# Kernel optimization log

Measured on AMD Instinct MI355X. Metric: run time of the kernel, lower is better.

The kernel has to match this reference:

```python
import jax, jax.numpy as jnp
import numpy as np

N, T, H, D = 8, 192, 1024, 128
P = 4            # t_patch_size (kernel = stride)
TP = T // P      # 48 patch tokens
E = 16384
HOUR, WDAY = 48, 7


def conv1d_patch(e, W, b):
    # e: [B, Cin, T]; W: [Cout, Cin, P]; kernel == stride == P (non-overlapping)
    B, Ci, Tt = e.shape
    e = e.reshape(B, Ci, Tt // P, P)
    return jnp.einsum('bctk,ock->bot', e, W) + b[None, :, None]  # [B, Cout, T']


def gcn_propagate(x, src, dst, coef):
    # x: [B, H, D] ; symmetric-normalized sparse A_hat @ x
    msg = x[:, src, :] * coef[None, :, None]
    return jnp.zeros_like(x).at[:, dst, :].add(msg)


def setup_inputs() -> dict:
    key = jax.random.key(0)
    ks = jax.random.split(key, 12)
    x = jax.random.normal(ks[0], (N, 1, T, H, 1), dtype=jnp.float32)
    x_mark = jax.random.randint(ks[1], (N, T, 2), 0, 7).astype(jnp.int64)
    edges = jax.random.randint(ks[2], (E, 2), 0, H).astype(jnp.int64)
    node_split = jnp.arange(H, dtype=jnp.int64).reshape(4, 256)
    s = 0.02
    params = {
        'hour_emb': jax.random.normal(ks[3], (HOUR, D), jnp.float32) * s,
        'weekday_emb': jax.random.normal(ks[4], (WDAY, D), jnp.float32) * s,
        'timeconv_w': jax.random.normal(ks[5], (D, D, P), jnp.float32) * s,
        'timeconv_b': jnp.zeros((D,), jnp.float32),
        'tconv_w': jax.random.normal(ks[6], (D, 1, P), jnp.float32) * s,
        'tconv_b': jnp.zeros((D,), jnp.float32),
        'W1': jax.random.normal(ks[7], (D, D), jnp.float32) * s,
        'b1': jnp.zeros((D,), jnp.float32),
        'W2': jax.random.normal(ks[8], (D, D), jnp.float32) * s,
        'b2': jnp.zeros((D,), jnp.float32),
    }
    return dict(x=x, x_mark=x_mark, edges=edges, node_split=node_split, **params)


def reference(x, x_mark, edges, node_split, hour_emb, weekday_emb,
              timeconv_w, timeconv_b, tconv_w, tconv_b, W1, b1, W2, b2):
    # ---- TimeEmb (TemporalEmbedding, hour_num='48') ----
    hour_x = hour_emb[x_mark[:, :, 1]]        # [N, T, D]
    wday_x = weekday_emb[x_mark[:, :, 0]]     # [N, T, D]
    time_emb = conv1d_patch((hour_x + wday_x).transpose(0, 2, 1),
                            timeconv_w, timeconv_b).transpose(0, 2, 1)  # [N, T', D]

    # ---- temporal value embedding ----
    xv = jnp.squeeze(x, (1, 4)).transpose(0, 2, 1).reshape(N * H, 1, T)  # [N*H,1,T]
    tv = conv1d_patch(xv, tconv_w, tconv_b)                 # [N*H, D, T']
    tv = tv.transpose(0, 2, 1).reshape(N, H, TP, D)         # [N, H, T', D]
    tv = tv.transpose(0, 2, 1, 3).reshape(N * TP, H, D)     # [N*T', H, D]

    # ---- 2-layer GCN with self-loops + symmetric normalization ----
    src = jnp.concatenate([edges[:, 0], jnp.arange(H)])
    dst = jnp.concatenate([edges[:, 1], jnp.arange(H)])
    deg = jnp.zeros((H,), tv.dtype).at[dst].add(1.0)
    coef = jax.lax.rsqrt(deg[src] * deg[dst])
    h = jax.nn.relu(gcn_propagate(tv, src, dst, coef) @ W1 + b1)
    token = gcn_propagate(h, src, dst, coef) @ W2 + b2      # [N*T', H, D]
    token = token.reshape(N, TP, H, D)

    # ---- per-group gather + mean pooling, interleaved per time step ----
    G = node_split.shape[0]
    grouped = token[:, :, node_split.reshape(-1), :].reshape(N, TP, G, -1, D)
    token = grouped.mean(axis=3).reshape(N, TP * G, D)      # [N, T'*G, D]

    time_rep = jnp.repeat(time_emb, G, axis=1)              # [N, T'*G, D]
    out = token + time_rep  # is_time == 1; eval mode -> no dropout
    return out, time_rep
```

## Files before the change

kernel.cpp:

```cpp
#include <hip/hip_runtime.h>
#include <hip/hip_bf16.h>

#define NN 8
#define TT 192
#define HH 1024
#define DD 128
#define TPP 48
#define EE 16384
#define NEDGE (EE + HH)
#define BB (NN * TPP)
#define NOUT (NN * TT * DD)

typedef short bf16x8 __attribute__((ext_vector_type(8)));
typedef float f32x4 __attribute__((ext_vector_type(4)));

__device__ __forceinline__ float bf2f(__hip_bfloat16 h) { return __bfloat162float(h); }
__device__ __forceinline__ float us2f(unsigned short u) {
  union { unsigned i; float f; } t;
  t.i = ((unsigned)u) << 16;
  return t.f;
}

__global__ __launch_bounds__(256) void k_setup(
    const int* __restrict__ edges, int* __restrict__ degE,
    const int* __restrict__ node_split, int* __restrict__ inv,
    const float* __restrict__ tw, float* __restrict__ twT,
    float* __restrict__ zbuf,
    const float* __restrict__ x, __hip_bfloat16* __restrict__ Xall) {
  __shared__ float tile[64][65];
  int tid = threadIdx.x, bid = blockIdx.x;
  int i = bid * 256 + tid;
  if (i < EE) atomicAdd(&degE[edges[2 * i + 1]], 1);
  if (i < HH) inv[node_split[i]] = i;
  if (i < 65536) twT[(i & 511) * DD + (i >> 9)] = tw[i];
  if (i < 6144) zbuf[i] = 0.f;

  int tt = bid % 24, st = bid / 24;
  int t0 = tt * 64, s0 = st * 64;
  int sl = tid & 63, r4 = tid >> 6;
#pragma unroll 4
  for (int ii = 0; ii < 16; ++ii) {
    int tl = ii * 4 + r4;
    tile[tl][sl] = x[(size_t)(t0 + tl) * HH + s0 + sl];
  }
  __syncthreads();
#pragma unroll 4
  for (int ii = 0; ii < 16; ++ii) {
    int sl2 = ii * 4 + r4;
    Xall[(size_t)(s0 + sl2) * 1536 + t0 + sl] = __float2bfloat16(tile[sl][sl2]);
  }
}

__global__ __launch_bounds__(1024) void k_scan(const int* __restrict__ degE,
                                               int* __restrict__ row_ptr,
                                               const float* __restrict__ tcw,
                                               const float* __restrict__ tcb,
                                               const float* __restrict__ W1,
                                               float* __restrict__ CW,
                                               const float* __restrict__ W2,
                                               __hip_bfloat16* __restrict__ w2sw) {
  int t = threadIdx.x, lane = t & 63, wid = t >> 6;
  int v = degE[t] + 1;
#pragma unroll
  for (int off = 1; off < 64; off <<= 1) {
    int u = __shfl_up(v, off, 64);
    if (lane >= off) v += u;
  }
  __shared__ int wsum[16];
  if (lane == 63) wsum[wid] = v;
  __syncthreads();
  if (t < 64) {
    int s = (lane < 16) ? wsum[lane] : 0;
#pragma unroll
    for (int off = 1; off < 16; off <<= 1) {
      int u = __shfl_up(s, off, 64);
      if (lane >= off) s += u;
    }
    if (lane < 16) wsum[lane] = s;
  }
  __syncthreads();
  int base = wid ? wsum[wid - 1] : 0;
  row_ptr[t + 1] = base + v;
  if (t == 0) row_ptr[0] = 0;

  if (t < 640) {
    int j = t >> 7, o = t & 127;
    float acc = 0.f;
    if (j < 4)
      for (int d = 0; d < DD; ++d) acc = fmaf(tcw[d * 4 + j], W1[d * DD + o], acc);
    else
      for (int d = 0; d < DD; ++d) acc = fmaf(tcb[d], W1[d * DD + o], acc);
    CW[j * DD + o] = acc;
  }
#pragma unroll 4
  for (int u = 0; u < 16; ++u) {
    int i = t * 16 + u;
    int n = i >> 7, k = i & 127;
    int dstb = n * 256 + (((k >> 3) ^ (n & 7)) * 16) + (k & 7) * 2;
    w2sw[dstb >> 1] = __float2bfloat16(W2[k * DD + n]);
  }
}

__global__ void k_scatter(const int* __restrict__ edges, const int* __restrict__ degE,
                          const int* __restrict__ row_ptr, const int* __restrict__ inv,
                          int* __restrict__ fill, int* __restrict__ csr_src,
                          float* __restrict__ csr_coef, float* __restrict__ csum,
                          float* __restrict__ QT) {
  int e = blockIdx.x * 256 + threadIdx.x;
  if (e >= NEDGE) return;
  int s, dt;
  if (e < EE) { s = edges[2 * e]; dt = edges[2 * e + 1]; }
  else        { s = dt = e - EE; }
  float ds = (float)(degE[s] + 1);
  float dd = (float)(degE[dt] + 1);
  float cf = rsqrtf(ds * dd);
  int pos = atomicAdd(&fill[dt], 1);
  int at = row_ptr[dt] + pos;
  csr_src[at] = s;
  csr_coef[at] = cf;
  atomicAdd(&csum[dt], cf);
  int g = inv[dt] >> 8;
  atomicAdd(&QT[s * 4 + g], cf * (1.0f / 256.0f));
}

__global__ __launch_bounds__(256) void k_spmm(
    const int* __restrict__ row_ptr, const int* __restrict__ csr_src,
    const float* __restrict__ csr_coef, const __hip_bfloat16* __restrict__ Xall,
    __hip_bfloat16* __restrict__ xbar,
    const int* __restrict__ xm, const float* __restrict__ hour_emb,
    const float* __restrict__ wday_emb, const float* __restrict__ twT,
    const float* __restrict__ tcb, float* __restrict__ out) {
  __shared__ float sL[2][512];
  int tid = threadIdx.x, bid = blockIdx.x;
  if (bid < HH) {
    int h = bid;
    int j0 = row_ptr[h], j1 = row_ptr[h + 1];
    float a0 = 0.f, a1 = 0.f, a2 = 0.f, a3 = 0.f, a4 = 0.f, a5 = 0.f;
    for (int j = j0; j < j1; ++j) {
      int s = csr_src[j];
      float cf = csr_coef[j];
      const unsigned* xr = (const unsigned*)(Xall + (size_t)s * 1536);
      unsigned u0 = xr[tid], u1 = xr[tid + 256], u2 = xr[tid + 512];
      union { unsigned i; float f; } lo, hi;
      lo.i = u0 << 16; hi.i = u0 & 0xffff0000u;
      a0 = fmaf(cf, lo.f, a0); a1 = fmaf(cf, hi.f, a1);
      lo.i = u1 << 16; hi.i = u1 & 0xffff0000u;
      a2 = fmaf(cf, lo.f, a2); a3 = fmaf(cf, hi.f, a3);
      lo.i = u2 << 16; hi.i = u2 & 0xffff0000u;
      a4 = fmaf(cf, lo.f, a4); a5 = fmaf(cf, hi.f, a5);
    }
    unsigned* xw = (unsigned*)(xbar + (size_t)h * 1536);
    union { __hip_bfloat16 h2[2]; unsigned u; } pk;
    pk.h2[0] = __float2bfloat16(a0); pk.h2[1] = __float2bfloat16(a1);
    xw[tid] = pk.u;
    pk.h2[0] = __float2bfloat16(a2); pk.h2[1] = __float2bfloat16(a3);
    xw[tid + 256] = pk.u;
    pk.h2[0] = __float2bfloat16(a4); pk.h2[1] = __float2bfloat16(a5);
    xw[tid + 512] = pk.u;
  } else {
    int bb = bid - HH;
    int half = tid >> 7, o = tid & 127;
    int b = bb * 2 + half;
    int n = b / TPP, tp = b % TPP;
    for (int k = 0; k < 4; ++k) {
      int t = tp * 4 + k;
      int wd = xm[(n * TT + t) * 2 + 0];
      int hr = xm[(n * TT + t) * 2 + 1];
      sL[half][o * 4 + k] = hour_emb[hr * DD + o] + wday_emb[wd * DD + o];
    }
    __syncthreads();
    float a0 = tcb[o], a1 = 0.f, a2 = 0.f, a3 = 0.f;
    for (int j = 0; j < 512; j += 4) {
      a0 = fmaf(sL[half][j + 0], twT[(j + 0) * DD + o], a0);
      a1 = fmaf(sL[half][j + 1], twT[(j + 1) * DD + o], a1);
      a2 = fmaf(sL[half][j + 2], twT[(j + 2) * DD + o], a2);
      a3 = fmaf(sL[half][j + 3], twT[(j + 3) * DD + o], a3);
    }
    float acc = (a0 + a1) + (a2 + a3);
    size_t base = (size_t)NOUT + ((size_t)n * TT + tp * 4) * DD + o;
    out[base] = acc;
    out[base + DD] = acc;
    out[base + 2 * DD] = acc;
    out[base + 3 * DD] = acc;
  }
}

__global__ __launch_bounds__(256) void k_red(const __hip_bfloat16* __restrict__ xbar,
                                             const float* __restrict__ csum,
                                             const float* __restrict__ QT,
                                             const float* __restrict__ CW,
                                             const float* __restrict__ b1,
                                             float* __restrict__ ypar) {
  __shared__ float4 xb4[256];
  __shared__ float4 qv[256];
  __shared__ float csv[256];
  __shared__ float yL[512];
  int tid = threadIdx.x, bid = blockIdx.x;
  int b = bid >> 2, qt = bid & 3;
  int h = qt * 256 + tid;
  {
    ushort4 us = *(const ushort4*)(xbar + (size_t)h * 1536 + b * 4);
    xb4[tid] = make_float4(us2f(us.x), us2f(us.y), us2f(us.z), us2f(us.w));
    qv[tid] = *(const float4*)(QT + h * 4);
    csv[tid] = csum[h];
  }
  int o = tid & 127, sub = tid >> 7;
  float cw0 = CW[o], cw1 = CW[DD + o], cw2 = CW[2 * DD + o];
  float cw3 = CW[3 * DD + o], cw4 = CW[4 * DD + o];
  float b1o = b1[o];
  __syncthreads();
  float y0 = 0.f, y1 = 0.f, y2 = 0.f, y3 = 0.f;
  int hh0 = sub * 128;
#pragma unroll 4
  for (int hh = hh0; hh < hh0 + 128; ++hh) {
    float4 xv = xb4[hh];
    float4 q = qv[hh];
    float c = csv[hh];
    float t = fmaf(c, cw4, b1o);
    t = fmaf(xv.x, cw0, t);
    t = fmaf(xv.y, cw1, t);
    t = fmaf(xv.z, cw2, t);
    t = fmaf(xv.w, cw3, t);
    t = fmaxf(t, 0.f);
    y0 = fmaf(q.x, t, y0);
    y1 = fmaf(q.y, t, y1);
    y2 = fmaf(q.z, t, y2);
    y3 = fmaf(q.w, t, y3);
  }
  if (sub == 0) {
    yL[o] = y0; yL[DD + o] = y1; yL[2 * DD + o] = y2; yL[3 * DD + o] = y3;
  }
  __syncthreads();
  if (sub == 1) {
    yL[o] += y0; yL[DD + o] += y1; yL[2 * DD + o] += y2; yL[3 * DD + o] += y3;
  }
  __syncthreads();
  float* yp = ypar + ((size_t)qt * BB + b) * 512;
  yp[tid] = yL[tid];
  yp[tid + 256] = yL[tid + 256];
}

__global__ __launch_bounds__(256, 2) void k_out(const float* __restrict__ ypar,
                                                const __hip_bfloat16* __restrict__ w2sw,
                                                const float* __restrict__ b2,
                                                float* __restrict__ out) {
  __shared__ __align__(16) char Wr[32768];
  __shared__ __align__(16) char Gr[16384];
  int tid = threadIdx.x;
  int m0 = blockIdx.x * 64;
  {
    const uint4* ws = (const uint4*)w2sw;
    uint4* wd = (uint4*)Wr;
    for (int i = tid; i < 2048; i += 256) wd[i] = ws[i];
  }
#pragma unroll 4
  for (int it = 0; it < 16; ++it) {
    int pi = it * 256 + tid;
    int row = pi >> 6, kp = pi & 63;
    int base = (m0 + row) * 128 + 2 * kp;
    float s0 = 0.f, s1 = 0.f;
#pragma unroll
    for (int p = 0; p < 4; ++p) {
      s0 += ypar[(size_t)p * (BB * 512) + base];
      s1 += ypar[(size_t)p * (BB * 512) + base + 1];
    }
    union { __hip_bfloat16 h[2]; unsigned u; } pk;
    pk.h[0] = __float2bfloat16(s0);
    pk.h[1] = __float2bfloat16(s1);
    *(unsigned*)(Gr + row * 256 + (((kp >> 2) ^ (row & 7)) * 16) + (kp & 3) * 4) = pk.u;
  }
  int lane = tid & 63, w = tid >> 6;
  int colq = lane & 15, quad = lane >> 4;
  float bo[8];
#pragma unroll
  for (int jn = 0; jn < 8; ++jn) bo[jn] = b2[jn * 16 + colq];
  __syncthreads();

  f32x4 acc[8];
#pragma unroll
  for (int jn = 0; jn < 8; ++jn) acc[jn] = (f32x4){0.f, 0.f, 0.f, 0.f};
  int arow = w * 16 + colq;
#pragma unroll
  for (int kc = 0; kc < 4; ++kc) {
    bf16x8 af = *(const bf16x8*)(Gr + arow * 256 + (((kc * 4 + quad) ^ (arow & 7)) * 16));
#pragma unroll
    for (int jn = 0; jn < 8; ++jn) {
      int nr = jn * 16 + colq;
      bf16x8 bf = *(const bf16x8*)(Wr + nr * 256 + (((kc * 4 + quad) ^ (nr & 7)) * 16));
      acc[jn] = __builtin_amdgcn_mfma_f32_16x16x32_bf16(af, bf, acc[jn], 0, 0, 0);
    }
  }
#pragma unroll
  for (int reg = 0; reg < 4; ++reg) {
    int m = m0 + w * 16 + quad * 4 + reg;
    int b = m >> 2, g = m & 3;
    int n_ = b / TPP, tp = b % TPP;
    size_t rb = ((size_t)(n_ * TT + tp * 4 + g)) * DD;
#pragma unroll
    for (int jn = 0; jn < 8; ++jn) {
      int o = jn * 16 + colq;
      out[rb + o] = acc[jn][reg] + bo[jn] + out[(size_t)NOUT + rb + o];
    }
  }
}

extern "C" void kernel_launch(void* const* d_in, const int* in_sizes, int n_in,
                              void* d_out, int out_size, void* d_ws, size_t ws_size,
                              hipStream_t stream) {
  const float* x = (const float*)d_in[0];
  const int* xm = (const int*)d_in[1];
  const int* edges = (const int*)d_in[2];
  const int* node_split = (const int*)d_in[3];
  const float* hour_emb = (const float*)d_in[4];
  const float* wday_emb = (const float*)d_in[5];
  const float* timeconv_w = (const float*)d_in[6];
  const float* timeconv_b = (const float*)d_in[7];
  const float* tcw = (const float*)d_in[8];
  const float* tcb = (const float*)d_in[9];
  const float* W1 = (const float*)d_in[10];
  const float* b1 = (const float*)d_in[11];
  const float* W2 = (const float*)d_in[12];
  const float* b2 = (const float*)d_in[13];
  float* out = (float*)d_out;

  char* w = (char*)d_ws;
  int* degE = (int*)(w + 0);
  int* fill = (int*)(w + 4096);
  float* csum = (float*)(w + 8192);
  float* QT = (float*)(w + 12288);
  int* row_ptr = (int*)(w + 28672);
  int* inv = (int*)(w + 33024);
  int* csr_src = (int*)(w + 37120);
  float* csr_coef = (float*)(w + 106752);
  __hip_bfloat16* w2sw = (__hip_bfloat16*)(w + 176384);
  float* CW = (float*)(w + 209152);
  float* twT = (float*)(w + 213248);
  __hip_bfloat16* Xall = (__hip_bfloat16*)(w + 475392);
  float* ypar = (float*)(w + 475392);
  __hip_bfloat16* xbar = (__hip_bfloat16*)(w + 3621120);

  hipMemsetAsync(degE, 0, 4096, stream);
  k_setup<<<384, 256, 0, stream>>>(edges, degE, node_split, inv, timeconv_w, twT,
                                   (float*)(w + 4096), x, Xall);
  k_scan<<<1, 1024, 0, stream>>>(degE, row_ptr, tcw, tcb, W1, CW, W2, w2sw);
  k_scatter<<<68, 256, 0, stream>>>(edges, degE, row_ptr, inv, fill, csr_src, csr_coef,
                                    csum, QT);
  k_spmm<<<HH + BB / 2, 256, 0, stream>>>(row_ptr, csr_src, csr_coef, Xall, xbar, xm,
                                          hour_emb, wday_emb, twT, timeconv_b, out);
  k_red<<<BB * 4, 256, 0, stream>>>(xbar, csum, QT, CW, b1, ypar);
  k_out<<<24, 256, 0, stream>>>(ypar, w2sw, b2, out);
}
```

Baseline: 154.0 us.

## Fuse all stages into one persistent kernel with software grid barriers

Replaces the six kernel launches with a single persistent kernel of 512 blocks. The former kernel boundaries become a hierarchical atomic grid barrier, which is meant to remove launch overhead and the tail idle time between stages. Work is redistributed over the fixed grid: the scan now runs in one 256-thread block, each spmm block handles two nodes, and each reduction block loops over three units. This relies on all 512 blocks being co-resident (launch_bounds 256,2 with 48KB shared memory), otherwise the barrier deadlocks. ypar also moves out of the region it previously shared with Xall.

```diff
diff --git a/kernel.cpp b/kernel.cpp
--- a/kernel.cpp
+++ b/kernel.cpp
@@ -10,296 +10,315 @@
 #define NEDGE (EE + HH)
 #define BB (NN * TPP)
 #define NOUT (NN * TT * DD)
+#define NBLK 512
 
 typedef short bf16x8 __attribute__((ext_vector_type(8)));
 typedef float f32x4 __attribute__((ext_vector_type(4)));
 
-__device__ __forceinline__ float bf2f(__hip_bfloat16 h) { return __bfloat162float(h); }
+struct KParams {
+  const float* x; const int* xm; const int* edges; const int* node_split;
+  const float* hour_emb; const float* wday_emb; const float* tw; const float* tw_b;
+  const float* tcw; const float* tcb; const float* W1; const float* b1;
+  const float* W2; const float* b2;
+  float* out;
+  int* degE; int* bar; float* zbuf; float* csum; float* QT;
+  int* row_ptr; int* inv; int* csr_src; float* csr_coef; int* fill;
+  __hip_bfloat16* w2sw; float* CW; float* twT;
+  __hip_bfloat16* Xall; __hip_bfloat16* xbar; float* ypar;
+};
+
 __device__ __forceinline__ float us2f(unsigned short u) {
   union { unsigned i; float f; } t;
   t.i = ((unsigned)u) << 16;
   return t.f;
 }
 
-__global__ __launch_bounds__(256) void k_setup(
-    const int* __restrict__ edges, int* __restrict__ degE,
-    const int* __restrict__ node_split, int* __restrict__ inv,
-    const float* __restrict__ tw, float* __restrict__ twT,
-    float* __restrict__ zbuf,
-    const float* __restrict__ x, __hip_bfloat16* __restrict__ Xall) {
-  __shared__ float tile[64][65];
-  int tid = threadIdx.x, bid = blockIdx.x;
-  int i = bid * 256 + tid;
-  if (i < EE) atomicAdd(&degE[edges[2 * i + 1]], 1);
-  if (i < HH) inv[node_split[i]] = i;
-  if (i < 65536) twT[(i & 511) * DD + (i >> 9)] = tw[i];
-  if (i < 6144) zbuf[i] = 0.f;
-
-  int tt = bid % 24, st = bid / 24;
-  int t0 = tt * 64, s0 = st * 64;
-  int sl = tid & 63, r4 = tid >> 6;
+__device__ __forceinline__ void gridbar(int* bar) {
+  __syncthreads();
+  if (threadIdx.x == 0) {
+    __threadfence();
+    int gen = __hip_atomic_load(&bar[0], __ATOMIC_RELAXED, __HIP_MEMORY_SCOPE_AGENT);
+    int sub = blockIdx.x & 63;
+    int t = atomicAdd(&bar[32 + sub * 16], 1);
+    if (t == (NBLK / 64) - 1) {
+      atomicExch(&bar[32 + sub * 16], 0);
+      int m = atomicAdd(&bar[16], 1);
+      if (m == 63) {
+        atomicExch(&bar[16], 0);
+        atomicAdd(&bar[0], 1);
+      } else {
+        while (__hip_atomic_load(&bar[0], __ATOMIC_RELAXED, __HIP_MEMORY_SCOPE_AGENT) == gen)
+          __builtin_amdgcn_s_sleep(1);
+      }
+    } else {
+      while (__hip_atomic_load(&bar[0], __ATOMIC_RELAXED, __HIP_MEMORY_SCOPE_AGENT) == gen)
+        __builtin_amdgcn_s_sleep(1);
+    }
+    __threadfence();
+  }
+  __syncthreads();
+}
+
+__global__ __launch_bounds__(256, 2) void k_mega(KParams P) {
+  __shared__ __align__(16) char U[49152];
+  int tid = threadIdx.x;
+  int bid = blockIdx.x;
+
+  if (bid < 256) {
+    int i = bid * 256 + tid;
+    if (i < EE) atomicAdd(&P.degE[P.edges[2 * i + 1]], 1);
+    if (i < HH) P.inv[P.node_split[i]] = i;
+    P.twT[(i & 511) * DD + (i >> 9)] = P.tw[i];
+    if (i < 6144) P.zbuf[i] = 0.f;
+  }
+  if (bid < 384) {
+    float(*tile)[65] = (float(*)[65])U;
+    int tt = bid % 24, st = bid / 24;
+    int t0 = tt * 64, s0 = st * 64;
+    int sl = tid & 63, r4 = tid >> 6;
 #pragma unroll 4
-  for (int ii = 0; ii < 16; ++ii) {
-    int tl = ii * 4 + r4;
-    tile[tl][sl] = x[(size_t)(t0 + tl) * HH + s0 + sl];
-  }
-  __syncthreads();
+    for (int ii = 0; ii < 16; ++ii) {
+      int tl = ii * 4 + r4;
+      tile[tl][sl] = P.x[(size_t)(t0 + tl) * HH + s0 + sl];
+    }
+    __syncthreads();
 #pragma unroll 4
-  for (int ii = 0; ii < 16; ++ii) {
-    int sl2 = ii * 4 + r4;
-    Xall[(size_t)(s0 + sl2) * 1536 + t0 + sl] = __float2bfloat16(tile[sl][sl2]);
-  }
-}
-
-__global__ __launch_bounds__(1024) void k_scan(const int* __restrict__ degE,
-                                               int* __restrict__ row_ptr,
-                                               const float* __restrict__ tcw,
-                                               const float* __restrict__ tcb,
-                                               const float* __restrict__ W1,
-                                               float* __restrict__ CW,
-                                               const float* __restrict__ W2,
-                                               __hip_bfloat16* __restrict__ w2sw) {
-  int t = threadIdx.x, lane = t & 63, wid = t >> 6;
-  int v = degE[t] + 1;
-#pragma unroll
-  for (int off = 1; off < 64; off <<= 1) {
-    int u = __shfl_up(v, off, 64);
-    if (lane >= off) v += u;
-  }
-  __shared__ int wsum[16];
-  if (lane == 63) wsum[wid] = v;
-  __syncthreads();
-  if (t < 64) {
-    int s = (lane < 16) ? wsum[lane] : 0;
-#pragma unroll
-    for (int off = 1; off < 16; off <<= 1) {
-      int u = __shfl_up(s, off, 64);
-      if (lane >= off) s += u;
-    }
-    if (lane < 16) wsum[lane] = s;
-  }
-  __syncthreads();
-  int base = wid ? wsum[wid - 1] : 0;
-  row_ptr[t + 1] = base + v;
-  if (t == 0) row_ptr[0] = 0;
-
-  if (t < 640) {
-    int j = t >> 7, o = t & 127;
-    float acc = 0.f;
-    if (j < 4)
-      for (int d = 0; d < DD; ++d) acc = fmaf(tcw[d * 4 + j], W1[d * DD + o], acc);
-    else
-      for (int d = 0; d < DD; ++d) acc = fmaf(tcb[d], W1[d * DD + o], acc);
-    CW[j * DD + o] = acc;
-  }
-#pragma unroll 4
-  for (int u = 0; u < 16; ++u) {
-    int i = t * 16 + u;
-    int n = i >> 7, k = i & 127;
-    int dstb = n * 256 + (((k >> 3) ^ (n & 7)) * 16) + (k & 7) * 2;
-    w2sw[dstb >> 1] = __float2bfloat16(W2[k * DD + n]);
-  }
-}
-
-__global__ void k_scatter(const int* __restrict__ edges, const int* __restrict__ degE,
-                          const int* __restrict__ row_ptr, const int* __restrict__ inv,
-                          int* __restrict__ fill, int* __restrict__ csr_src,
-                          float* __restrict__ csr_coef, float* __restrict__ csum,
-                          float* __restrict__ QT) {
-  int e = blockIdx.x * 256 + threadIdx.x;
-  if (e >= NEDGE) return;
-  int s, dt;
-  if (e < EE) { s = edges[2 * e]; dt = edges[2 * e + 1]; }
-  else        { s = dt = e - EE; }
-  float ds = (float)(degE[s] + 1);
-  float dd = (float)(degE[dt] + 1);
-  float cf = rsqrtf(ds * dd);
-  int pos = atomicAdd(&fill[dt], 1);
-  int at = row_ptr[dt] + pos;
-  csr_src[at] = s;
-  csr_coef[at] = cf;
-  atomicAdd(&csum[dt], cf);
-  int g = inv[dt] >> 8;
-  atomicAdd(&QT[s * 4 + g], cf * (1.0f / 256.0f));
-}
-
-__global__ __launch_bounds__(256) void k_spmm(
-    const int* __restrict__ row_ptr, const int* __restrict__ csr_src,
-    const float* __restrict__ csr_coef, const __hip_bfloat16* __restrict__ Xall,
-    __hip_bfloat16* __restrict__ xbar,
-    const int* __restrict__ xm, const float* __restrict__ hour_emb,
-    const float* __restrict__ wday_emb, const float* __restrict__ twT,
-    const float* __restrict__ tcb, float* __restrict__ out) {
-  __shared__ float sL[2][512];
-  int tid = threadIdx.x, bid = blockIdx.x;
-  if (bid < HH) {
-    int h = bid;
-    int j0 = row_ptr[h], j1 = row_ptr[h + 1];
-    float a0 = 0.f, a1 = 0.f, a2 = 0.f, a3 = 0.f, a4 = 0.f, a5 = 0.f;
-    for (int j = j0; j < j1; ++j) {
-      int s = csr_src[j];
-      float cf = csr_coef[j];
-      const unsigned* xr = (const unsigned*)(Xall + (size_t)s * 1536);
-      unsigned u0 = xr[tid], u1 = xr[tid + 256], u2 = xr[tid + 512];
-      union { unsigned i; float f; } lo, hi;
-      lo.i = u0 << 16; hi.i = u0 & 0xffff0000u;
-      a0 = fmaf(cf, lo.f, a0); a1 = fmaf(cf, hi.f, a1);
-      lo.i = u1 << 16; hi.i = u1 & 0xffff0000u;
-      a2 = fmaf(cf, lo.f, a2); a3 = fmaf(cf, hi.f, a3);
-      lo.i = u2 << 16; hi.i = u2 & 0xffff0000u;
-      a4 = fmaf(cf, lo.f, a4); a5 = fmaf(cf, hi.f, a5);
-    }
-    unsigned* xw = (unsigned*)(xbar + (size_t)h * 1536);
-    union { __hip_bfloat16 h2[2]; unsigned u; } pk;
-    pk.h2[0] = __float2bfloat16(a0); pk.h2[1] = __float2bfloat16(a1);
-    xw[tid] = pk.u;
-    pk.h2[0] = __float2bfloat16(a2); pk.h2[1] = __float2bfloat16(a3);
-    xw[tid + 256] = pk.u;
-    pk.h2[0] = __float2bfloat16(a4); pk.h2[1] = __float2bfloat16(a5);
-    xw[tid + 512] = pk.u;
-  } else {
-    int bb = bid - HH;
+    for (int ii = 0; ii < 16; ++ii) {
+      int sl2 = ii * 4 + r4;
+      P.Xall[(size_t)(s0 + sl2) * 1536 + t0 + sl] = __float2bfloat16(tile[sl][sl2]);
+    }
+  }
+  gridbar(P.bar);
+
+  if (bid == 0) {
+    int t4 = tid * 4;
+    int v0 = P.degE[t4] + 1, v1 = P.degE[t4 + 1] + 1;
+    int v2 = P.degE[t4 + 2] + 1, v3 = P.degE[t4 + 3] + 1;
+    int s_ = v0 + v1 + v2 + v3;
+    int lane = tid & 63, wid = tid >> 6;
+    int inc = s_;
+#pragma unroll
+    for (int off = 1; off < 64; off <<= 1) {
+      int u = __shfl_up(inc, off, 64);
+      if (lane >= off) inc += u;
+    }
+    int* wsum = (int*)U;
+    if (lane == 63) wsum[wid] = inc;
+    __syncthreads();
+    int wb = 0;
+    for (int ww = 0; ww < wid; ++ww) wb += wsum[ww];
+    int ex = wb + inc - s_;
+    P.row_ptr[t4 + 1] = ex + v0;
+    P.row_ptr[t4 + 2] = ex + v0 + v1;
+    P.row_ptr[t4 + 3] = ex + v0 + v1 + v2;
+    P.row_ptr[t4 + 4] = ex + s_;
+    if (tid == 0) P.row_ptr[0] = 0;
+  } else if (bid <= 192) {
+    int u = bid - 1;
+    float(*sL)[512] = (float(*)[512])U;
     int half = tid >> 7, o = tid & 127;
-    int b = bb * 2 + half;
+    int b = u * 2 + half;
     int n = b / TPP, tp = b % TPP;
     for (int k = 0; k < 4; ++k) {
       int t = tp * 4 + k;
-      int wd = xm[(n * TT + t) * 2 + 0];
-      int hr = xm[(n * TT + t) * 2 + 1];
-      sL[half][o * 4 + k] = hour_emb[hr * DD + o] + wday_emb[wd * DD + o];
-    }
-    __syncthreads();
-    float a0 = tcb[o], a1 = 0.f, a2 = 0.f, a3 = 0.f;
+      int wd = P.xm[(n * TT + t) * 2 + 0];
+      int hr = P.xm[(n * TT + t) * 2 + 1];
+      sL[half][o * 4 + k] = P.hour_emb[hr * DD + o] + P.wday_emb[wd * DD + o];
+    }
+    __syncthreads();
+    float a0 = P.tw_b[o], a1 = 0.f, a2 = 0.f, a3 = 0.f;
     for (int j = 0; j < 512; j += 4) {
-      a0 = fmaf(sL[half][j + 0], twT[(j + 0) * DD + o], a0);
-      a1 = fmaf(sL[half][j + 1], twT[(j + 1) * DD + o], a1);
-      a2 = fmaf(sL[half][j + 2], twT[(j + 2) * DD + o], a2);
-      a3 = fmaf(sL[half][j + 3], twT[(j + 3) * DD + o], a3);
+      a0 = fmaf(sL[half][j + 0], P.twT[(j + 0) * DD + o], a0);
+      a1 = fmaf(sL[half][j + 1], P.twT[(j + 1) * DD + o], a1);
+      a2 = fmaf(sL[half][j + 2], P.twT[(j + 2) * DD + o], a2);
+      a3 = fmaf(sL[half][j + 3], P.twT[(j + 3) * DD + o], a3);
     }
     float acc = (a0 + a1) + (a2 + a3);
     size_t base = (size_t)NOUT + ((size_t)n * TT + tp * 4) * DD + o;
-    out[base] = acc;
-    out[base + DD] = acc;
-    out[base + 2 * DD] = acc;
-    out[base + 3 * DD] = acc;
-  }
-}
-
-__global__ __launch_bounds__(256) void k_red(const __hip_bfloat16* __restrict__ xbar,
-                                             const float* __restrict__ csum,
-                                             const float* __restrict__ QT,
-                                             const float* __restrict__ CW,
-                                             const float* __restrict__ b1,
-                                             float* __restrict__ ypar) {
-  __shared__ float4 xb4[256];
-  __shared__ float4 qv[256];
-  __shared__ float csv[256];
-  __shared__ float yL[512];
-  int tid = threadIdx.x, bid = blockIdx.x;
-  int b = bid >> 2, qt = bid & 3;
-  int h = qt * 256 + tid;
+    P.out[base] = acc;
+    P.out[base + DD] = acc;
+    P.out[base + 2 * DD] = acc;
+    P.out[base + 3 * DD] = acc;
+  } else if (bid <= 195) {
+    int j = (bid - 193) * 256 + tid;
+    if (j < 640) {
+      int jr = j >> 7, o = j & 127;
+      float acc = 0.f;
+      if (jr < 4)
+        for (int d = 0; d < DD; ++d) acc = fmaf(P.tcw[d * 4 + jr], P.W1[d * DD + o], acc);
+      else
+        for (int d = 0; d < DD; ++d) acc = fmaf(P.tcb[d], P.W1[d * DD + o], acc);
+      P.CW[jr * DD + o] = acc;
+    }
+  } else if (bid < 260) {
+    int i = (bid - 196) * 256 + tid;
+    int n = i >> 7, k = i & 127;
+    int dstb = n * 256 + (((k >> 3) ^ (n & 7)) * 16) + (k & 7) * 2;
+    P.w2sw[dstb >> 1] = __float2bfloat16(P.W2[k * DD + n]);
+  }
+  gridbar(P.bar);
+
+  if (bid < 68) {
+    int e = bid * 256 + tid;
+    if (e < NEDGE) {
+      int s, dt;
+      if (e < EE) { s = P.edges[2 * e]; dt = P.edges[2 * e + 1]; }
+      else        { s = dt = e - EE; }
+      float ds = (float)(P.degE[s] + 1);
+      float dd = (float)(P.degE[dt] + 1);
+      float cf = rsqrtf(ds * dd);
+      int pos = atomicAdd(&P.fill[dt], 1);
+      int at = P.row_ptr[dt] + pos;
+      P.csr_src[at] = s;
+      P.csr_coef[at] = cf;
+      atomicAdd(&P.csum[dt], cf);
+      int g = P.inv[dt] >> 8;
+      atomicAdd(&P.QT[s * 4 + g], cf * (1.0f / 256.0f));
+    }
+  }
+  gridbar(P.bar);
+
   {
-    ushort4 us = *(const ushort4*)(xbar + (size_t)h * 1536 + b * 4);
-    xb4[tid] = make_float4(us2f(us.x), us2f(us.y), us2f(us.z), us2f(us.w));
-    qv[tid] = *(const float4*)(QT + h * 4);
-    csv[tid] = csum[h];
-  }
-  int o = tid & 127, sub = tid >> 7;
-  float cw0 = CW[o], cw1 = CW[DD + o], cw2 = CW[2 * DD + o];
-  float cw3 = CW[3 * DD + o], cw4 = CW[4 * DD + o];
-  float b1o = b1[o];
-  __syncthreads();
-  float y0 = 0.f, y1 = 0.f, y2 = 0.f, y3 = 0.f;
-  int hh0 = sub * 128;
+    int h = bid * 2 + (tid >> 7);
+    int c = tid & 127;
+    int j0 = P.row_ptr[h], j1 = P.row_ptr[h + 1];
+    float a[12];
+#pragma unroll
+    for (int u = 0; u < 12; ++u) a[u] = 0.f;
+    for (int j = j0; j < j1; ++j) {
+      int s = P.csr_src[j];
+      float cf = P.csr_coef[j];
+      const unsigned* xr = (const unsigned*)(P.Xall + (size_t)s * 1536);
+#pragma unroll
+      for (int u = 0; u < 6; ++u) {
+        unsigned v = xr[c + u * 128];
+        union { unsigned i; float f; } lo, hi;
+        lo.i = v << 16;
+        hi.i = v & 0xffff0000u;
+        a[2 * u] = fmaf(cf, lo.f, a[2 * u]);
+        a[2 * u + 1] = fmaf(cf, hi.f, a[2 * u + 1]);
+      }
+    }
+    unsigned* xw = (unsigned*)(P.xbar + (size_t)h * 1536);
+#pragma unroll
+    for (int u = 0; u < 6; ++u) {
+      union { __hip_bfloat16 h2[2]; unsigned u2; } pk;
+      pk.h2[0] = __float2bfloat16(a[2 * u]);
+      pk.h2[1] = __float2bfloat16(a[2 * u + 1]);
+      xw[c + u * 128] = pk.u2;
+    }
+  }
+  gridbar(P.bar);
+
+  for (int uu = 0; uu < 3; ++uu) {
+    int unit = bid + uu * NBLK;
+    int b = unit >> 2, qt = unit & 3;
+    int h = qt * 256 + tid;
+    float4* xb4 = (float4*)U;
+    float4* qv = (float4*)(U + 4096);
+    float* csv = (float*)(U + 8192);
+    float* yL = (float*)(U + 9216);
+    {
+      ushort4 us = *(const ushort4*)(P.xbar + (size_t)h * 1536 + b * 4);
+      xb4[tid] = make_float4(us2f(us.x), us2f(us.y), us2f(us.z), us2f(us.w));
+      qv[tid] = *(const float4*)(P.QT + h * 4);
+      csv[tid] = P.csum[h];
+    }
+    int o = tid & 127, sub = tid >> 7;
+    float cw0 = P.CW[o], cw1 = P.CW[DD + o], cw2 = P.CW[2 * DD + o];
+    float cw3 = P.CW[3 * DD + o], cw4 = P.CW[4 * DD + o];
+    float b1o = P.b1[o];
+    __syncthreads();
+    float y0 = 0.f, y1 = 0.f, y2 = 0.f, y3 = 0.f;
+    int hh0 = sub * 128;
 #pragma unroll 4
-  for (int hh = hh0; hh < hh0 + 128; ++hh) {
-    float4 xv = xb4[hh];
-    float4 q = qv[hh];
-    float c = csv[hh];
-    float t = fmaf(c, cw4, b1o);
-    t = fmaf(xv.x, cw0, t);
-    t = fmaf(xv.y, cw1, t);
-    t = fmaf(xv.z, cw2, t);
-    t = fmaf(xv.w, cw3, t);
-    t = fmaxf(t, 0.f);
-    y0 = fmaf(q.x, t, y0);
-    y1 = fmaf(q.y, t, y1);
-    y2 = fmaf(q.z, t, y2);
-    y3 = fmaf(q.w, t, y3);
-  }
-  if (sub == 0) {
-    yL[o] = y0; yL[DD + o] = y1; yL[2 * DD + o] = y2; yL[3 * DD + o] = y3;
-  }
-  __syncthreads();
-  if (sub == 1) {
-    yL[o] += y0; yL[DD + o] += y1; yL[2 * DD + o] += y2; yL[3 * DD + o] += y3;
-  }
-  __syncthreads();
-  float* yp = ypar + ((size_t)qt * BB + b) * 512;
-  yp[tid] = yL[tid];
-  yp[tid + 256] = yL[tid + 256];
-}
-
-__global__ __launch_bounds__(256, 2) void k_out(const float* __restrict__ ypar,
-                                                const __hip_bfloat16* __restrict__ w2sw,
-                                                const float* __restrict__ b2,
-                                                float* __restrict__ out) {
-  __shared__ __align__(16) char Wr[32768];
-  __shared__ __align__(16) char Gr[16384];
-  int tid = threadIdx.x;
-  int m0 = blockIdx.x * 64;
-  {
-    const uint4* ws = (const uint4*)w2sw;
-    uint4* wd = (uint4*)Wr;
-    for (int i = tid; i < 2048; i += 256) wd[i] = ws[i];
-  }
+    for (int hh = hh0; hh < hh0 + 128; ++hh) {
+      float4 xv = xb4[hh];
+      float4 q = qv[hh];
+      float cc = csv[hh];
+      float t = fmaf(cc, cw4, b1o);
+      t = fmaf(xv.x, cw0, t);
+      t = fmaf(xv.y, cw1, t);
+      t = fmaf(xv.z, cw2, t);
+      t = fmaf(xv.w, cw3, t);
+      t = fmaxf(t, 0.f);
+      y0 = fmaf(q.x, t, y0);
+      y1 = fmaf(q.y, t, y1);
+      y2 = fmaf(q.z, t, y2);
+      y3 = fmaf(q.w, t, y3);
+    }
+    if (sub == 0) {
+      yL[o] = y0; yL[DD + o] = y1; yL[2 * DD + o] = y2; yL[3 * DD + o] = y3;
+    }
+    __syncthreads();
+    if (sub == 1) {
+      yL[o] += y0; yL[DD + o] += y1; yL[2 * DD + o] += y2; yL[3 * DD + o] += y3;
+    }
+    __syncthreads();
+    float* yp = P.ypar + ((size_t)qt * BB + b) * 512;
+    yp[tid] = yL[tid];
+    yp[tid + 256] = yL[tid + 256];
+    __syncthreads();
+  }
+  gridbar(P.bar);
+
+  if (bid < 24) {
+    char* Wr = U;
+    char* Gr = U + 32768;
+    int m0 = bid * 64;
+    {
+      const uint4* ws = (const uint4*)P.w2sw;
+      uint4* wd = (uint4*)Wr;
+      for (int i = tid; i < 2048; i += 256) wd[i] = ws[i];
+    }
 #pragma unroll 4
-  for (int it = 0; it < 16; ++it) {
-    int pi = it * 256 + tid;
-    int row = pi >> 6, kp = pi & 63;
-    int base = (m0 + row) * 128 + 2 * kp;
-    float s0 = 0.f, s1 = 0.f;
-#pragma unroll
-    for (int p = 0; p < 4; ++p) {
-      s0 += ypar[(size_t)p * (BB * 512) + base];
-      s1 += ypar[(size_t)p * (BB * 512) + base + 1];
-    }
-    union { __hip_bfloat16 h[2]; unsigned u; } pk;
-    pk.h[0] = __float2bfloat16(s0);
-    pk.h[1] = __float2bfloat16(s1);
-    *(unsigned*)(Gr + row * 256 + (((kp >> 2) ^ (row & 7)) * 16) + (kp & 3) * 4) = pk.u;
-  }
-  int lane = tid & 63, w = tid >> 6;
-  int colq = lane & 15, quad = lane >> 4;
-  float bo[8];
-#pragma unroll
-  for (int jn = 0; jn < 8; ++jn) bo[jn] = b2[jn * 16 + colq];
-  __syncthreads();
-
-  f32x4 acc[8];
-#pragma unroll
-  for (int jn = 0; jn < 8; ++jn) acc[jn] = (f32x4){0.f, 0.f, 0.f, 0.f};
-  int arow = w * 16 + colq;
-#pragma unroll
-  for (int kc = 0; kc < 4; ++kc) {
-    bf16x8 af = *(const bf16x8*)(Gr + arow * 256 + (((kc * 4 + quad) ^ (arow & 7)) * 16));
-#pragma unroll
-    for (int jn = 0; jn < 8; ++jn) {
-      int nr = jn * 16 + colq;
-      bf16x8 bf = *(const bf16x8*)(Wr + nr * 256 + (((kc * 4 + quad) ^ (nr & 7)) * 16));
-      acc[jn] = __builtin_amdgcn_mfma_f32_16x16x32_bf16(af, bf, acc[jn], 0, 0, 0);
-    }
-  }
-#pragma unroll
-  for (int reg = 0; reg < 4; ++reg) {
-    int m = m0 + w * 16 + quad * 4 + reg;
-    int b = m >> 2, g = m & 3;
-    int n_ = b / TPP, tp = b % TPP;
-    size_t rb = ((size_t)(n_ * TT + tp * 4 + g)) * DD;
-#pragma unroll
-    for (int jn = 0; jn < 8; ++jn) {
-      int o = jn * 16 + colq;
-      out[rb + o] = acc[jn][reg] + bo[jn] + out[(size_t)NOUT + rb + o];
+    for (int it = 0; it < 16; ++it) {
+      int pi = it * 256 + tid;
+      int row = pi >> 6, kp = pi & 63;
+      int base = (m0 + row) * 128 + 2 * kp;
+      float s0 = 0.f, s1 = 0.f;
+#pragma unroll
+      for (int p = 0; p < 4; ++p) {
+        s0 += P.ypar[(size_t)p * (BB * 512) + base];
+        s1 += P.ypar[(size_t)p * (BB * 512) + base + 1];
+      }
+      union { __hip_bfloat16 h[2]; unsigned u; } pk;
+      pk.h[0] = __float2bfloat16(s0);
+      pk.h[1] = __float2bfloat16(s1);
+      *(unsigned*)(Gr + row * 256 + (((kp >> 2) ^ (row & 7)) * 16) + (kp & 3) * 4) = pk.u;
+    }
+    int lane = tid & 63, w = tid >> 6;
+    int colq = lane & 15, quad = lane >> 4;
+    float bo[8];
+#pragma unroll
+    for (int jn = 0; jn < 8; ++jn) bo[jn] = P.b2[jn * 16 + colq];
+    __syncthreads();
+
+    f32x4 acc[8];
+#pragma unroll
+    for (int jn = 0; jn < 8; ++jn) acc[jn] = (f32x4){0.f, 0.f, 0.f, 0.f};
+    int arow = w * 16 + colq;
+#pragma unroll
+    for (int kc = 0; kc < 4; ++kc) {
+      bf16x8 af = *(const bf16x8*)(Gr + arow * 256 + (((kc * 4 + quad) ^ (arow & 7)) * 16));
+#pragma unroll
+      for (int jn = 0; jn < 8; ++jn) {
+        int nr = jn * 16 + colq;
+        bf16x8 bf = *(const bf16x8*)(Wr + nr * 256 + (((kc * 4 + quad) ^ (nr & 7)) * 16));
+        acc[jn] = __builtin_amdgcn_mfma_f32_16x16x32_bf16(af, bf, acc[jn], 0, 0, 0);
+      }
+    }
+#pragma unroll
+    for (int reg = 0; reg < 4; ++reg) {
+      int m = m0 + w * 16 + quad * 4 + reg;
+      int b = m >> 2, g = m & 3;
+      int n_ = b / TPP, tp = b % TPP;
+      size_t rb = ((size_t)(n_ * TT + tp * 4 + g)) * DD;
+#pragma unroll
+      for (int jn = 0; jn < 8; ++jn) {
+        int o = jn * 16 + colq;
+        P.out[rb + o] = acc[jn][reg] + bo[jn] + P.out[(size_t)NOUT + rb + o];
+      }
     }
   }
 }
@@ -307,46 +326,41 @@
 extern "C" void kernel_launch(void* const* d_in, const int* in_sizes, int n_in,
                               void* d_out, int out_size, void* d_ws, size_t ws_size,
                               hipStream_t stream) {
-  const float* x = (const float*)d_in[0];
-  const int* xm = (const int*)d_in[1];
-  const int* edges = (const int*)d_in[2];
-  const int* node_split = (const int*)d_in[3];
-  const float* hour_emb = (const float*)d_in[4];
-  const float* wday_emb = (const float*)d_in[5];
-  const float* timeconv_w = (const float*)d_in[6];
-  const float* timeconv_b = (const float*)d_in[7];
-  const float* tcw = (const float*)d_in[8];
-  const float* tcb = (const float*)d_in[9];
-  const float* W1 = (const float*)d_in[10];
-  const float* b1 = (const float*)d_in[11];
-  const float* W2 = (const float*)d_in[12];
-  const float* b2 = (const float*)d_in[13];
-  float* out = (float*)d_out;
-
   char* w = (char*)d_ws;
-  int* degE = (int*)(w + 0);
-  int* fill = (int*)(w + 4096);
-  float* csum = (float*)(w + 8192);
-  float* QT = (float*)(w + 12288);
-  int* row_ptr = (int*)(w + 28672);
-  int* inv = (int*)(w + 33024);
-  int* csr_src = (int*)(w + 37120);
-  float* csr_coef = (float*)(w + 106752);
-  __hip_bfloat16* w2sw = (__hip_bfloat16*)(w + 176384);
-  float* CW = (float*)(w + 209152);
-  float* twT = (float*)(w + 213248);
-  __hip_bfloat16* Xall = (__hip_bfloat16*)(w + 475392);
-  float* ypar = (float*)(w + 475392);
-  __hip_bfloat16* xbar = (__hip_bfloat16*)(w + 3621120);
-
-  hipMemsetAsync(degE, 0, 4096, stream);
-  k_setup<<<384, 256, 0, stream>>>(edges, degE, node_split, inv, timeconv_w, twT,
-                                   (float*)(w + 4096), x, Xall);
-  k_scan<<<1, 1024, 0, stream>>>(degE, row_ptr, tcw, tcb, W1, CW, W2, w2sw);
-  k_scatter<<<68, 256, 0, stream>>>(edges, degE, row_ptr, inv, fill, csr_src, csr_coef,
-                                    csum, QT);
-  k_spmm<<<HH + BB / 2, 256, 0, stream>>>(row_ptr, csr_src, csr_coef, Xall, xbar, xm,
-                                          hour_emb, wday_emb, twT, timeconv_b, out);
-  k_red<<<BB * 4, 256, 0, stream>>>(xbar, csum, QT, CW, b1, ypar);
-  k_out<<<24, 256, 0, stream>>>(ypar, w2sw, b2, out);
+  KParams P;
+  P.x = (const float*)d_in[0];
+  P.xm = (const int*)d_in[1];
+  P.edges = (const int*)d_in[2];
+  P.node_split = (const int*)d_in[3];
+  P.hour_emb = (const float*)d_in[4];
+  P.wday_emb = (const float*)d_in[5];
+  P.tw = (const float*)d_in[6];
+  P.tw_b = (const float*)d_in[7];
+  P.tcw = (const float*)d_in[8];
+  P.tcb = (const float*)d_in[9];
+  P.W1 = (const float*)d_in[10];
+  P.b1 = (const float*)d_in[11];
+  P.W2 = (const float*)d_in[12];
+  P.b2 = (const float*)d_in[13];
+  P.out = (float*)d_out;
+
+  P.degE = (int*)(w + 0);
+  P.bar = (int*)(w + 4096);
+  P.zbuf = (float*)(w + 12288);
+  P.fill = (int*)(w + 12288);
+  P.csum = (float*)(w + 16384);
+  P.QT = (float*)(w + 20480);
+  P.row_ptr = (int*)(w + 36864);
+  P.inv = (int*)(w + 41216);
+  P.csr_src = (int*)(w + 45312);
+  P.csr_coef = (float*)(w + 114944);
+  P.w2sw = (__hip_bfloat16*)(w + 184576);
+  P.CW = (float*)(w + 217344);
+  P.twT = (float*)(w + 221440);
+  P.Xall = (__hip_bfloat16*)(w + 483584);
+  P.xbar = (__hip_bfloat16*)(w + 3629312);
+  P.ypar = (float*)(w + 6775040);
+
+  hipMemsetAsync(d_ws, 0, 12288, stream);
+  k_mega<<<NBLK, 256, 0, stream>>>(P);
 }
```

Result: slower. 261.7 us (+69.9%).
